# Kernel optimization log

Measured on AMD Instinct MI355X. Metric: run time of the kernel, lower is better.

Reference implementation:

```python
import jax, jax.numpy as jnp
import numpy as np

B, N, D, H = 8, 577, 768, 12
HD = D // H
SCALE = HD ** -0.5
LN_EPS = 1e-5


def layer_norm(x, w, b):
    mu = jnp.mean(x, -1, keepdims=True)
    var = jnp.mean((x - mu) ** 2, -1, keepdims=True)
    return (x - mu) * jax.lax.rsqrt(var + LN_EPS) * w + b


def wasserstein_distance_matmul(mean1, cov1, mean2, cov2):
    # all [B,H,N,hd]; returns [B,H,N,N]
    m1_2 = jnp.sum(mean1 ** 2, -1, keepdims=True)
    m2_2 = jnp.sum(mean2 ** 2, -1, keepdims=True)
    ret = -2.0 * jnp.einsum('bhnd,bhmd->bhnm', mean1, mean2) + m1_2 + jnp.swapaxes(m2_2, -1, -2)
    c1s = jnp.sqrt(jnp.clip(cov1, 1e-24))
    c2s = jnp.sqrt(jnp.clip(cov2, 1e-24))
    cov_ret = (-2.0 * jnp.einsum('bhnd,bhmd->bhnm', c1s, c2s)
               + jnp.sum(cov1, -1, keepdims=True)
               + jnp.swapaxes(jnp.sum(cov2, -1, keepdims=True), -1, -2))
    return ret + cov_ret


def setup_inputs() -> dict:
    key = jax.random.key(0)
    ks = jax.random.split(key, 20)
    s = 0.02
    return {
        'x_mean': jax.random.normal(ks[0], (B, N, D), jnp.float32),
        'x_cov': jax.random.normal(ks[1], (B, N, D), jnp.float32),
        'rel_pos_bias': jax.random.normal(ks[2], (1, H, N, N), jnp.float32),
        'norm1_w': jnp.ones((D,), jnp.float32),
        'norm1_b': jnp.zeros((D,), jnp.float32),
        'qkv_w': jax.random.normal(ks[3], (3 * D, D), jnp.float32) * s,
        'proj_w': jax.random.normal(ks[4], (D, D), jnp.float32) * s,
        'proj_b': jnp.zeros((D,), jnp.float32),
        'cov_proj_w': jax.random.normal(ks[5], (D, D), jnp.float32) * s,
        'cov_proj_b': jnp.zeros((D,), jnp.float32),
        'norm2_w': jnp.ones((D,), jnp.float32),
        'norm2_b': jnp.zeros((D,), jnp.float32),
        'fc1_w': jax.random.normal(ks[6], (4 * D, D), jnp.float32) * s,
        'fc1_b': jnp.zeros((4 * D,), jnp.float32),
        'fc2_w': jax.random.normal(ks[7], (D, 4 * D), jnp.float32) * s,
        'fc2_b': jnp.zeros((D,), jnp.float32),
        'gamma1': 0.1 * jnp.ones((D,), jnp.float32),
        'gamma2': 0.1 * jnp.ones((D,), jnp.float32),
    }


def _split_heads(t):
    # [B,N,3D] -> q,k,v each [B,H,N,hd]
    t = t.reshape(B, N, 3, H, HD).transpose(2, 0, 3, 1, 4)
    return t[0], t[1], t[2]


def attention(xm, xc, rel_pos_bias, qkv_w, proj_w, proj_b, cov_proj_w, cov_proj_b):
    qkv = xm @ qkv_w.T                                  # [B,N,3D]
    q, k, v = _split_heads(qkv)
    cov_qkv = jax.nn.elu(xc @ qkv_w.T) + 1.0            # same weights for cov stream
    cov_q, cov_k, cov_v = _split_heads(cov_qkv)
    q = q * SCALE
    attn = -wasserstein_distance_matmul(q, cov_q, k, cov_k)
    attn = jax.nn.sigmoid(attn + 1e-24)
    attn = jax.nn.softmax(attn + rel_pos_bias, axis=-1)  # [B,H,N,N]
    mean_ctx = jnp.einsum('bhnm,bhmd->bhnd', attn, v).transpose(0, 2, 1, 3).reshape(B, N, D)
    cov_ctx = jnp.einsum('bhnm,bhmd->bhnd', attn ** 2, cov_v).transpose(0, 2, 1, 3).reshape(B, N, D)
    mean_out = mean_ctx @ proj_w.T + proj_b
    cov_out = cov_ctx @ cov_proj_w.T + cov_proj_b
    return mean_out, cov_out


def mlp(x, fc1_w, fc1_b, fc2_w, fc2_b):
    h = jax.nn.gelu(x @ fc1_w.T + fc1_b, approximate=False)
    return h @ fc2_w.T + fc2_b


def reference(x_mean, x_cov, rel_pos_bias, norm1_w, norm1_b, qkv_w, proj_w, proj_b,
              cov_proj_w, cov_proj_b, norm2_w, norm2_b, fc1_w, fc1_b, fc2_w, fc2_b,
              gamma1, gamma2):
    mean, cov = attention(layer_norm(x_mean, norm1_w, norm1_b),
                          layer_norm(x_cov, norm1_w, norm1_b),
                          rel_pos_bias, qkv_w, proj_w, proj_b, cov_proj_w, cov_proj_b)
    x_mean = x_mean + gamma1 * mean
    fcm = gamma2 * mlp(layer_norm(x_mean, norm2_w, norm2_b), fc1_w, fc1_b, fc2_w, fc2_b)
    x_cov = x_cov + gamma1 * cov
    fcc = gamma2 * mlp(layer_norm(x_cov, norm2_w, norm2_b), fc1_w, fc1_b, fc2_w, fc2_b)
    return (x_mean + fcm, x_cov + fcc)
```

## Files before the change

### kernel.cpp

```cpp
#include <hip/hip_runtime.h>
#include <hip/hip_bf16.h>
#include <math.h>
#include <stdint.h>

typedef __bf16 bf16;
typedef __attribute__((ext_vector_type(8))) __bf16 bf16x8;
typedef __attribute__((ext_vector_type(4))) float f32x4;

typedef __attribute__((address_space(1))) void gas_void;
typedef __attribute__((address_space(3))) void las_void;

#define DEV __device__ __forceinline__

static constexpr int B_ = 8, N_ = 577, D_ = 768, H_ = 12;
static constexpr int M_ = B_ * N_;
static constexpr int MP_ = 4736;
static constexpr int NP_ = 640;
static constexpr int BH_ = B_ * H_;
static constexpr float SCALE_ = 0.125f;

DEV void async_cp16(const void* g, void* l) {
  __builtin_amdgcn_global_load_lds((gas_void*)g, (las_void*)l, 16, 0, 0);
}
DEV float fast_rcp(float x) { return __builtin_amdgcn_rcpf(x); }
DEV float elu1(float x) { return x > 0.0f ? x + 1.0f : __expf(x); }
DEV float fast_gelu(float x) {
  const float x2 = x * x;
  const float z = x * fmaf(0.0713548826f, x2, 1.5957691216f);
  return x * fast_rcp(1.0f + __expf(-z));
}

__global__ __launch_bounds__(256) void cvt6_kernel(
    const float* __restrict__ s0, const float* __restrict__ s1,
    const float* __restrict__ s2, const float* __restrict__ s3,
    const float* __restrict__ s4, const float* __restrict__ s5,
    bf16* __restrict__ d0, bf16* __restrict__ d1, bf16* __restrict__ d2,
    bf16* __restrict__ d3, bf16* __restrict__ d4, bf16* __restrict__ d5,
    int n0, int n1, int n2, int n3, int n4c, int n5) {
  const float* ss[6] = {s0, s1, s2, s3, s4, s5};
  bf16* dd[6] = {d0, d1, d2, d3, d4, d5};
  const int nn[6] = {n0, n1, n2, n3, n4c, n5};
  int bid = blockIdx.x;
  int seg = 0;
#pragma unroll 6
  for (int k = 0; k < 6; k++) {
    const int nb = (nn[k] + 255) >> 8;
    if (bid < nb) { seg = k; break; }
    bid -= nb;
  }
  const int i = bid * 256 + threadIdx.x;
  if (i < nn[seg]) {
    const float4 v = ((const float4*)ss[seg])[i];
    bf16 o[4] = {(bf16)v.x, (bf16)v.y, (bf16)v.z, (bf16)v.w};
    *(uint64_t*)(dd[seg] + (size_t)i * 4) = *(const uint64_t*)o;
  }
}

__global__ __launch_bounds__(256) void ln2_kernel(
    const float* __restrict__ x0, const float* __restrict__ x1,
    const float* __restrict__ w, const float* __restrict__ bp,
    bf16* __restrict__ out) {
  const int row = blockIdx.x;
  const int st = (int)(row >= M_);
  const int srow = row - st * M_;
  const float* xr = (st ? x1 : x0) + (size_t)srow * D_;
  const int t = threadIdx.x;
  float v0 = xr[t], v1 = xr[t + 256], v2 = xr[t + 512];
  float s = v0 + v1 + v2;
  float ss = v0 * v0 + v1 * v1 + v2 * v2;
#pragma unroll
  for (int m = 32; m >= 1; m >>= 1) {
    s += __shfl_down(s, m);
    ss += __shfl_down(ss, m);
  }
  __shared__ float red[8];
  if ((t & 63) == 0) { red[t >> 6] = s; red[4 + (t >> 6)] = ss; }
  __syncthreads();
  s = red[0] + red[1] + red[2] + red[3];
  ss = red[4] + red[5] + red[6] + red[7];
  const float mu = s * (1.0f / D_);
  float var = ss * (1.0f / D_) - mu * mu;
  var = fmaxf(var, 0.0f);
  const float rs = rsqrtf(var + 1e-5f);
  bf16* orow = out + ((size_t)st * MP_ + srow) * D_;
  orow[t]       = (bf16)((v0 - mu) * rs * w[t]       + bp[t]);
  orow[t + 256] = (bf16)((v1 - mu) * rs * w[t + 256] + bp[t + 256]);
  orow[t + 512] = (bf16)((v2 - mu) * rs * w[t + 512] + bp[t + 512]);
}

enum { EP_BF16 = 0, EP_PROJ = 1, EP_GELU = 2, EP_FC2 = 3 };

template <int EP, int K>
__global__ __launch_bounds__(256) void gemm_bt(
    const bf16* __restrict__ A, const bf16* __restrict__ W0,
    const bf16* __restrict__ W1, int Nn, int gx,
    const float* __restrict__ bias0, const float* __restrict__ bias1,
    const float* __restrict__ gamma,
    const float* __restrict__ resid0, const float* __restrict__ resid1,
    bf16* __restrict__ Cb, float* __restrict__ Cf0, float* __restrict__ Cf1) {
  __shared__ __align__(16) bf16 As[3][128 * 32];
  __shared__ __align__(16) bf16 Bs[3][128 * 32];
  const int nwg = gridDim.x;
  const int o = blockIdx.x;
  const int q = nwg >> 3, r = nwg & 7, xcd = o & 7;
  const int flat = (xcd < r ? xcd * (q + 1) : r * (q + 1) + (xcd - r) * q) + (o >> 3);
  const int bx = flat % gx, by = flat / gx;

  const int t = threadIdx.x;
  const int lane = t & 63, wv = t >> 6;
  const int ln = lane & 15, kg = lane >> 4;
  const int wr = wv >> 1, wc = wv & 1;
  const int s = (int)(by >= (MP_ / 128));
  const bf16* W = s ? W1 : W0;
  const size_t brow = (size_t)by * 128;
  const size_t bcol = (size_t)bx * 128;
  const int r0 = t >> 2, gsl = t & 3;
  const bf16* A0 = A + (brow + r0) * (size_t)K + gsl * 8;
  const bf16* A1 = A + (brow + r0 + 64) * (size_t)K + gsl * 8;
  const bf16* W0p = W + (bcol + r0) * (size_t)K + gsl * 8;
  const bf16* W1p = W + (bcol + r0 + 64) * (size_t)K + gsl * 8;

  auto stage = [&](int buf, int kk) {
    async_cp16(A0 + kk, &As[buf][(wv * 64) * 8]);
    async_cp16(A1 + kk, &As[buf][(256 + wv * 64) * 8]);
    async_cp16(W0p + kk, &Bs[buf][(wv * 64) * 8]);
    async_cp16(W1p + kk, &Bs[buf][(256 + wv * 64) * 8]);
  };

  f32x4 acc[4][4] = {};
  constexpr int nt = K >> 5;
  static_assert(nt % 3 == 0, "K/32 must be divisible by 3");
  stage(0, 0);
  stage(1, 32);
#pragma unroll 1
  for (int tb = 0; tb < nt; tb += 3) {
#pragma unroll
    for (int u = 0; u < 3; u++) {
      const int tt = tb + u;
      if (tt + 1 < nt) {
        asm volatile("s_waitcnt vmcnt(4)" ::: "memory");
      } else {
        asm volatile("s_waitcnt vmcnt(0)" ::: "memory");
      }
      __builtin_amdgcn_s_barrier();
      bf16x8 af[4], bfr[4];
#pragma unroll
      for (int i = 0; i < 4; i++)
        af[i] = *(const bf16x8*)&As[u][(wr * 64 + i * 16 + ln) * 32 + kg * 8];
#pragma unroll
      for (int j = 0; j < 4; j++)
        bfr[j] = *(const bf16x8*)&Bs[u][(wc * 64 + j * 16 + ln) * 32 + kg * 8];
#pragma unroll
      for (int i = 0; i < 4; i++)
#pragma unroll
        for (int j = 0; j < 4; j++)
          acc[i][j] = __builtin_amdgcn_mfma_f32_16x16x32_bf16(af[i], bfr[j], acc[i][j], 0, 0, 0);
      if (tt + 2 < nt) stage((u + 2) % 3, (tt + 2) * 32);
    }
  }

  const float* biasS = s ? bias1 : bias0;
  const float* residS = s ? resid1 : resid0;
  float* CfS = s ? Cf1 : Cf0;
#pragma unroll
  for (int i = 0; i < 4; i++) {
    const int rb = (int)brow + wr * 64 + i * 16 + kg * 4;
#pragma unroll
    for (int j = 0; j < 4; j++) {
      const int col = (int)bcol + wc * 64 + j * 16 + ln;
#pragma unroll
      for (int rr = 0; rr < 4; rr++) {
        const int row = rb + rr;
        float v = acc[i][j][rr];
        if (EP == EP_BF16) {
          Cb[(size_t)row * Nn + col] = (bf16)v;
        } else if (EP == EP_GELU) {
          v += biasS[col];
          Cb[(size_t)row * Nn + col] = (bf16)fast_gelu(v);
        } else {
          const int r2 = row - s * MP_;
          if (r2 < M_) {
            v += biasS[col];
            if (EP == EP_PROJ) {
              CfS[(size_t)r2 * Nn + col] = residS[(size_t)r2 * Nn + col] + gamma[col] * v;
            } else {
              CfS[(size_t)r2 * Nn + col] += gamma[col] * v;
            }
          }
        }
      }
    }
  }
}

__global__ __launch_bounds__(256) void prep_kernel(
    const bf16* __restrict__ qm, const bf16* __restrict__ qc,
    bf16* __restrict__ Qcat, bf16* __restrict__ Kcat,
    bf16* __restrict__ Vt, bf16* __restrict__ CVt,
    float* __restrict__ rowt, float* __restrict__ colt) {
  const int n0 = blockIdx.x * 64;
  const int h = blockIdx.y, b = blockIdx.z;
  const int bh = b * H_ + h;
  const int t = threadIdx.x;
  const int nl = t >> 2, c = t & 3;
  const int n = n0 + nl;
  const bool valid = n < N_;
  __shared__ bf16 vts[64][72], cvts[64][72];
  float q2 = 0.f, cqs = 0.f, k2 = 0.f, cks = 0.f;
  bf16 qo[16], sqo[16], ko[16], sko[16];
  if (valid) {
    const size_t ro = (size_t)(b * N_ + n) * 2304 + h * 64 + c * 16;
#pragma unroll
    for (int half = 0; half < 2; half++) {
      bf16x8 qv8 = *(const bf16x8*)(qm + ro + half * 8);
      bf16x8 kv8 = *(const bf16x8*)(qm + ro + 768 + half * 8);
      bf16x8 vv8 = *(const bf16x8*)(qm + ro + 1536 + half * 8);
      bf16x8 cq8 = *(const bf16x8*)(qc + ro + half * 8);
      bf16x8 ck8 = *(const bf16x8*)(qc + ro + 768 + half * 8);
      bf16x8 cv8 = *(const bf16x8*)(qc + ro + 1536 + half * 8);
#pragma unroll
      for (int i = 0; i < 8; i++) {
        const int d = half * 8 + i;
        float qv = (float)qv8[i] * SCALE_;
        float kv = (float)kv8[i];
        float cq1 = elu1((float)cq8[i]);
        float ck1 = elu1((float)ck8[i]);
        q2 += qv * qv; cqs += cq1; k2 += kv * kv; cks += ck1;
        qo[d] = (bf16)qv; sqo[d] = (bf16)sqrtf(fmaxf(cq1, 1e-24f));
        ko[d] = (bf16)kv; sko[d] = (bf16)sqrtf(fmaxf(ck1, 1e-24f));
        vts[nl][c * 16 + d] = vv8[i];
        cvts[nl][c * 16 + d] = (bf16)elu1((float)cv8[i]);
      }
    }
  } else {
#pragma unroll
    for (int d = 0; d < 16; d++) {
      qo[d] = (bf16)0.f; sqo[d] = (bf16)0.f; ko[d] = (bf16)0.f; sko[d] = (bf16)0.f;
      vts[nl][c * 16 + d] = (bf16)0.f; cvts[nl][c * 16 + d] = (bf16)0.f;
    }
  }
  {
    bf16* qrow = Qcat + ((size_t)bh * NP_ + n) * 128;
    bf16* krow = Kcat + ((size_t)bh * NP_ + n) * 128;
#pragma unroll
    for (int d = 0; d < 16; d++) {
      qrow[c * 16 + d] = qo[d];
      qrow[64 + c * 16 + d] = sqo[d];
      krow[c * 16 + d] = ko[d];
      krow[64 + c * 16 + d] = sko[d];
    }
  }
  float rt = q2 + cqs, ct = k2 + cks;
  rt += __shfl_xor(rt, 1); rt += __shfl_xor(rt, 2);
  ct += __shfl_xor(ct, 1); ct += __shfl_xor(ct, 2);
  if (c == 0) { rowt[(size_t)bh * NP_ + n] = rt; colt[(size_t)bh * NP_ + n] = ct; }
  __syncthreads();
  const int drow = t >> 2;
  const size_t vb = ((size_t)bh * 64 + drow) * NP_ + n0 + c * 16;
#pragma unroll
  for (int i = 0; i < 16; i++) {
    Vt[vb + i] = vts[c * 16 + i][drow];
    CVt[vb + i] = cvts[c * 16 + i][drow];
  }
}

__global__ __launch_bounds__(256) void attn_kernel(
    const bf16* __restrict__ Qcat, const bf16* __restrict__ Kcat,
    const bf16* __restrict__ Vt, const bf16* __restrict__ CVt,
    const float* __restrict__ rowt, const float* __restrict__ colt,
    const bf16* __restrict__ bias,
    bf16* __restrict__ ctxm, bf16* __restrict__ ctxc) {
  const int id = blockIdx.x;
  const int xcd = id & 7, slot = id >> 3;
  const int g = xcd + 8 * (slot / 10);
  const int it = slot % 10;
  const int b = g / H_, h = g % H_;
  const int bh = g;
  const int i0 = it * 64;
  const int t = threadIdx.x;
  const int lane = t & 63, w = t >> 6;
  const int ln = lane & 15, kg = lane >> 4;
  __shared__ __align__(16) bf16 Ks[2][64 * 128];
  __shared__ __align__(16) bf16 Vs[2][64 * 64];
  __shared__ __align__(16) bf16 CVs[2][64 * 64];
  __shared__ __align__(16) bf16 Ps[64 * 72];

  const bf16* Qg = Qcat + (size_t)bh * NP_ * 128;
  const bf16* Kg = Kcat + (size_t)bh * NP_ * 128;
  const bf16* Vg = Vt + (size_t)bh * 64 * NP_;
  const bf16* CVg = CVt + (size_t)bh * 64 * NP_;

  auto stageK = [&](int buf, int j0) {
#pragma unroll
    for (int qq = 0; qq < 4; qq++) {
      const int idx = qq * 256 + t;
      const int row = idx >> 4, sl = idx & 15;
      async_cp16(Kg + (size_t)(j0 + row) * 128 + ((sl ^ (row & 7)) * 8),
                 &Ks[buf][(qq * 256 + w * 64) * 8]);
    }
  };
  auto stageV = [&](int buf, int j0) {
#pragma unroll
    for (int qq = 0; qq < 2; qq++) {
      const int idx = qq * 256 + t;
      const int row = idx >> 3, sl = idx & 7;
      async_cp16(Vg + (size_t)row * NP_ + j0 + ((sl ^ (row & 7)) * 8),
                 &Vs[buf][(qq * 256 + w * 64) * 8]);
      async_cp16(CVg + (size_t)row * NP_ + j0 + ((sl ^ (row & 7)) * 8),
                 &CVs[buf][(qq * 256 + w * 64) * 8]);
    }
  };

#pragma unroll
  for (int qq = 0; qq < 4; qq++) {
    const int idx = qq * 256 + t;
    const int row = idx >> 4, sl = idx & 15;
    async_cp16(Qg + (size_t)(i0 + row) * 128 + ((sl ^ (row & 7)) * 8),
               &Ks[0][(qq * 256 + w * 64) * 8]);
  }
  stageK(1, 0);
  stageV(0, 0);
  __syncthreads();
  bf16x8 aq[4];
  {
    const int row = w * 16 + ln;
#pragma unroll
    for (int kc = 0; kc < 4; kc++) {
      const int slot2 = kc * 4 + kg;
      aq[kc] = *(const bf16x8*)&Ks[0][row * 128 + ((slot2 ^ (row & 7)) * 8)];
    }
  }
  float rt[4];
#pragma unroll
  for (int r = 0; r < 4; r++) rt[r] = rowt[(size_t)bh * NP_ + i0 + w * 16 + kg * 4 + r];
  __syncthreads();

  f32x4 accm[4] = {}, accc[4] = {};
  float den[4] = {0.f, 0.f, 0.f, 0.f};
  const int igb = i0 + w * 16 + kg * 4;

  for (int jt = 0; jt < 10; jt++) {
    const int j0 = jt * 64;
    const int kc2 = (jt + 1) & 1;
    const int vc2 = jt & 1;
    if (jt + 1 < 10) {
      stageK(jt & 1, j0 + 64);
      stageV((jt + 1) & 1, j0 + 64);
    }
    float bb[4][4], ctb[4];
#pragma unroll
    for (int js = 0; js < 4; js++) {
      const int jg = j0 + js * 16 + ln;
      const int jc = jg < N_ ? jg : N_ - 1;
      ctb[js] = colt[(size_t)bh * NP_ + jg];
#pragma unroll
      for (int r = 0; r < 4; r++) {
        const int ic = (igb + r) < N_ ? (igb + r) : N_ - 1;
        bb[js][r] = (float)bias[((size_t)h * N_ + ic) * N_ + jc];
      }
    }
#pragma unroll
    for (int js = 0; js < 4; js++) {
      f32x4 sv = {};
#pragma unroll
      for (int kc = 0; kc < 4; kc++) {
        const int row = js * 16 + ln;
        const int slot2 = kc * 4 + kg;
        bf16x8 bk = *(const bf16x8*)&Ks[kc2][row * 128 + ((slot2 ^ (row & 7)) * 8)];
        sv = __builtin_amdgcn_mfma_f32_16x16x32_bf16(aq[kc], bk, sv, 0, 0, 0);
      }
      const int jg = j0 + js * 16 + ln;
#pragma unroll
      for (int r = 0; r < 4; r++) {
        const float S = 2.0f * sv[r] - rt[r] - ctb[js];
        const float sig = fast_rcp(1.0f + __expf(-S));
        float e = __expf(sig + bb[js][r]);
        if (jg >= N_) e = 0.0f;
        const bf16 eb = (bf16)e;
        den[r] += (float)eb;
        Ps[(w * 16 + kg * 4 + r) * 72 + js * 16 + ln] = eb;
      }
    }
#pragma unroll
    for (int ks = 0; ks < 2; ks++) {
      const int prow = w * 16 + ln;
      bf16x8 pa = *(const bf16x8*)&Ps[prow * 72 + ks * 32 + kg * 8];
      bf16x8 p2a;
#pragma unroll
      for (int i = 0; i < 8; i++) {
        const float pf = (float)pa[i];
        p2a[i] = (bf16)(pf * pf);
      }
#pragma unroll
      for (int nt = 0; nt < 4; nt++) {
        const int vrow = nt * 16 + ln;
        const int slot2 = ks * 4 + kg;
        bf16x8 vb = *(const bf16x8*)&Vs[vc2][vrow * 64 + ((slot2 ^ (vrow & 7)) * 8)];
        bf16x8 cvb = *(const bf16x8*)&CVs[vc2][vrow * 64 + ((slot2 ^ (vrow & 7)) * 8)];
        accm[nt] = __builtin_amdgcn_mfma_f32_16x16x32_bf16(pa, vb, accm[nt], 0, 0, 0);
        accc[nt] = __builtin_amdgcn_mfma_f32_16x16x32_bf16(p2a, cvb, accc[nt], 0, 0, 0);
      }
    }
    __syncthreads();
  }
#pragma unroll
  for (int r = 0; r < 4; r++) {
    float d = den[r];
    d += __shfl_xor(d, 1); d += __shfl_xor(d, 2);
    d += __shfl_xor(d, 4); d += __shfl_xor(d, 8);
    den[r] = d;
  }
#pragma unroll
  for (int r = 0; r < 4; r++) {
    const int ig = i0 + w * 16 + kg * 4 + r;
    if (ig < N_) {
      const float inv = fast_rcp(den[r]);
      const float inv2 = inv * inv;
      const size_t base = (size_t)(b * N_ + ig) * D_ + h * 64;
#pragma unroll
      for (int nt = 0; nt < 4; nt++) {
        ctxm[base + nt * 16 + ln] = (bf16)(accm[nt][r] * inv);
        ctxc[base + nt * 16 + ln] = (bf16)(accc[nt][r] * inv2);
      }
    }
  }
}

extern "C" void kernel_launch(void* const* d_in, const int* in_sizes, int n_in,
                              void* d_out, int out_size, void* d_ws, size_t ws_size,
                              hipStream_t stream) {
  const float* x_mean = (const float*)d_in[0];
  const float* x_cov  = (const float*)d_in[1];
  const float* rpb    = (const float*)d_in[2];
  const float* n1w    = (const float*)d_in[3];
  const float* n1b    = (const float*)d_in[4];
  const float* qkvw   = (const float*)d_in[5];
  const float* projw  = (const float*)d_in[6];
  const float* projb  = (const float*)d_in[7];
  const float* cprojw = (const float*)d_in[8];
  const float* cprojb = (const float*)d_in[9];
  const float* n2w    = (const float*)d_in[10];
  const float* n2b    = (const float*)d_in[11];
  const float* fc1w   = (const float*)d_in[12];
  const float* fc1b   = (const float*)d_in[13];
  const float* fc2w   = (const float*)d_in[14];
  const float* fc2b   = (const float*)d_in[15];
  const float* g1     = (const float*)d_in[16];
  const float* g2     = (const float*)d_in[17];
  (void)in_sizes; (void)n_in; (void)out_size; (void)ws_size;

  char* ws = (char*)d_ws;
  size_t off = 0;
  auto take = [&](size_t bytes) {
    char* p = ws + off;
    off += (bytes + 255) & ~(size_t)255;
    return p;
  };
  bf16* wq   = (bf16*)take((size_t)2304 * 768 * 2);
  bf16* wp   = (bf16*)take((size_t)768 * 768 * 2);
  bf16* wcp  = (bf16*)take((size_t)768 * 768 * 2);
  bf16* wf1  = (bf16*)take((size_t)3072 * 768 * 2);
  bf16* wf2  = (bf16*)take((size_t)768 * 3072 * 2);
  bf16* xln  = (bf16*)take((size_t)2 * MP_ * 768 * 2);
  char* R    = take((size_t)2 * MP_ * 3072 * 2);
  bf16* qkvb = (bf16*)R;
  bf16* hbuf = (bf16*)R;
  bf16* biasb = (bf16*)(R + (size_t)2 * MP_ * 2304 * 2);
  bf16* Qcat = (bf16*)take((size_t)BH_ * NP_ * 128 * 2);
  bf16* Kcat = (bf16*)take((size_t)BH_ * NP_ * 128 * 2);
  bf16* Vt   = (bf16*)take((size_t)BH_ * 64 * NP_ * 2);
  bf16* CVt  = (bf16*)take((size_t)BH_ * 64 * NP_ * 2);
  float* rowt = (float*)take((size_t)BH_ * NP_ * 4);
  float* colt = (float*)take((size_t)BH_ * NP_ * 4);
  bf16* ctx  = (bf16*)take((size_t)2 * MP_ * 768 * 2);

  float* outm = (float*)d_out;
  float* outc = outm + (size_t)M_ * D_;

  {
    const int c0 = 2304 * 768 / 4, c1 = 768 * 768 / 4, c2 = 768 * 768 / 4;
    const int c3 = 3072 * 768 / 4, c4 = 768 * 3072 / 4, c5 = H_ * N_ * N_ / 4;
    const int nb = ((c0 + 255) >> 8) + ((c1 + 255) >> 8) + ((c2 + 255) >> 8) +
                   ((c3 + 255) >> 8) + ((c4 + 255) >> 8) + ((c5 + 255) >> 8);
    cvt6_kernel<<<nb, 256, 0, stream>>>(qkvw, projw, cprojw, fc1w, fc2w, rpb,
                                        wq, wp, wcp, wf1, wf2, biasb,
                                        c0, c1, c2, c3, c4, c5);
  }
  ln2_kernel<<<2 * M_, 256, 0, stream>>>(x_mean, x_cov, n1w, n1b, xln);
  gemm_bt<EP_BF16, 768><<<18 * 74, 256, 0, stream>>>(xln, wq, wq, 2304, 18,
      nullptr, nullptr, nullptr, nullptr, nullptr, qkvb, nullptr, nullptr);
  prep_kernel<<<dim3(10, 12, 8), 256, 0, stream>>>(
      qkvb, qkvb + (size_t)MP_ * 2304, Qcat, Kcat, Vt, CVt, rowt, colt);
  attn_kernel<<<960, 256, 0, stream>>>(Qcat, Kcat, Vt, CVt, rowt, colt, biasb,
                                       ctx, ctx + (size_t)MP_ * 768);
  gemm_bt<EP_PROJ, 768><<<6 * 74, 256, 0, stream>>>(ctx, wp, wcp, 768, 6,
      projb, cprojb, g1, x_mean, x_cov, nullptr, outm, outc);
  ln2_kernel<<<2 * M_, 256, 0, stream>>>(outm, outc, n2w, n2b, xln);
  gemm_bt<EP_GELU, 768><<<24 * 74, 256, 0, stream>>>(xln, wf1, wf1, 3072, 24,
      fc1b, fc1b, nullptr, nullptr, nullptr, hbuf, nullptr, nullptr);
  gemm_bt<EP_FC2, 3072><<<6 * 74, 256, 0, stream>>>(hbuf, wf2, wf2, 768, 6,
      fc2b, fc2b, g2, nullptr, nullptr, nullptr, outm, outc);
}
```

Before: 371.6 us.

## Use double-buffered BK=64 GEMM tiles with XOR-swizzled LDS layout

The GEMM main loop moves from a triple-buffered K=32 pipeline with explicit vmcnt waits to a double-buffered K=64 pipeline with one __syncthreads per iteration. LDS tiles are stored with an XOR swizzle on the 16-byte chunk index, applied on the global source address side, to avoid bank conflicts on the fragment reads. This halves the number of barriers and raises the work per sync, at the cost of a shallower prefetch depth and a full-barrier wait that replaces the fine-grained vmcnt accounting.

```diff
diff --git a/kernel.cpp b/kernel.cpp
--- a/kernel.cpp
+++ b/kernel.cpp
@@ -98,8 +98,8 @@
     const float* __restrict__ gamma,
     const float* __restrict__ resid0, const float* __restrict__ resid1,
     bf16* __restrict__ Cb, float* __restrict__ Cf0, float* __restrict__ Cf1) {
-  __shared__ __align__(16) bf16 As[3][128 * 32];
-  __shared__ __align__(16) bf16 Bs[3][128 * 32];
+  __shared__ __align__(16) bf16 As[2][128 * 64];
+  __shared__ __align__(16) bf16 Bs[2][128 * 64];
   const int nwg = gridDim.x;
   const int o = blockIdx.x;
   const int q = nwg >> 3, r = nwg & 7, xcd = o & 7;
@@ -114,49 +114,49 @@
   const bf16* W = s ? W1 : W0;
   const size_t brow = (size_t)by * 128;
   const size_t bcol = (size_t)bx * 128;
-  const int r0 = t >> 2, gsl = t & 3;
-  const bf16* A0 = A + (brow + r0) * (size_t)K + gsl * 8;
-  const bf16* A1 = A + (brow + r0 + 64) * (size_t)K + gsl * 8;
-  const bf16* W0p = W + (bcol + r0) * (size_t)K + gsl * 8;
-  const bf16* W1p = W + (bcol + r0 + 64) * (size_t)K + gsl * 8;
+
+  const int rA = t >> 3, sl = t & 7;
+  const int swsl = (sl ^ (rA & 7)) * 8;
+  const bf16* Asrc = A + (brow + rA) * (size_t)K + swsl;
+  const bf16* Wsrc = W + (bcol + rA) * (size_t)K + swsl;
 
   auto stage = [&](int buf, int kk) {
-    async_cp16(A0 + kk, &As[buf][(wv * 64) * 8]);
-    async_cp16(A1 + kk, &As[buf][(256 + wv * 64) * 8]);
-    async_cp16(W0p + kk, &Bs[buf][(wv * 64) * 8]);
-    async_cp16(W1p + kk, &Bs[buf][(256 + wv * 64) * 8]);
+#pragma unroll
+    for (int q2 = 0; q2 < 4; q2++) {
+      async_cp16(Asrc + (size_t)q2 * 32 * K + kk, &As[buf][(q2 * 256 + wv * 64) * 8]);
+      async_cp16(Wsrc + (size_t)q2 * 32 * K + kk, &Bs[buf][(q2 * 256 + wv * 64) * 8]);
+    }
   };
 
   f32x4 acc[4][4] = {};
-  constexpr int nt = K >> 5;
-  static_assert(nt % 3 == 0, "K/32 must be divisible by 3");
+  constexpr int nt = K >> 6;
+  static_assert(K % 64 == 0, "K must be a multiple of 64");
   stage(0, 0);
-  stage(1, 32);
+  __syncthreads();
 #pragma unroll 1
-  for (int tb = 0; tb < nt; tb += 3) {
-#pragma unroll
-    for (int u = 0; u < 3; u++) {
-      const int tt = tb + u;
-      if (tt + 1 < nt) {
-        asm volatile("s_waitcnt vmcnt(4)" ::: "memory");
-      } else {
-        asm volatile("s_waitcnt vmcnt(0)" ::: "memory");
-      }
-      __builtin_amdgcn_s_barrier();
+  for (int tt = 0; tt < nt; ++tt) {
+    if (tt + 1 < nt) stage((tt + 1) & 1, (tt + 1) * 64);
+    const int bb = tt & 1;
+#pragma unroll
+    for (int kh = 0; kh < 2; kh++) {
       bf16x8 af[4], bfr[4];
 #pragma unroll
-      for (int i = 0; i < 4; i++)
-        af[i] = *(const bf16x8*)&As[u][(wr * 64 + i * 16 + ln) * 32 + kg * 8];
-#pragma unroll
-      for (int j = 0; j < 4; j++)
-        bfr[j] = *(const bf16x8*)&Bs[u][(wc * 64 + j * 16 + ln) * 32 + kg * 8];
+      for (int i = 0; i < 4; i++) {
+        const int row = wr * 64 + i * 16 + ln;
+        af[i] = *(const bf16x8*)&As[bb][row * 64 + (((kh * 4 + kg) ^ (ln & 7)) * 8)];
+      }
+#pragma unroll
+      for (int j = 0; j < 4; j++) {
+        const int row = wc * 64 + j * 16 + ln;
+        bfr[j] = *(const bf16x8*)&Bs[bb][row * 64 + (((kh * 4 + kg) ^ (ln & 7)) * 8)];
+      }
 #pragma unroll
       for (int i = 0; i < 4; i++)
 #pragma unroll
         for (int j = 0; j < 4; j++)
           acc[i][j] = __builtin_amdgcn_mfma_f32_16x16x32_bf16(af[i], bfr[j], acc[i][j], 0, 0, 0);
-      if (tt + 2 < nt) stage((u + 2) % 3, (tt + 2) * 32);
-    }
+    }
+    __syncthreads();
   }
 
   const float* biasS = s ? bias1 : bias0;
```

Result: faster. 348.5 us (-6.2%).
